# Kernel optimization log

Measured on AMD Instinct MI355X. Metric: run time of the kernel, lower is better.

Reference implementation:

```python
import jax, jax.numpy as jnp
import numpy as np

# Thresholds from PointsGeneration.__init__ defaults
THRES_TEXT = 0.45
THRES_HEAD = 0.5
THRES_BOND = 0.5

H = W = 2048


def setup_inputs() -> dict:
    key = jax.random.key(0)
    ks = jax.random.split(key, 7)
    mk = lambda k, c: jax.random.normal(k, (1, c, H, W), dtype=jnp.float32)
    return {
        "score_text": mk(ks[0], 1),
        "score_head": mk(ks[1], 1),
        "score_tail": mk(ks[2], 1),
        "score_bond": mk(ks[3], 1),
        "reg_head": mk(ks[4], 4),
        "reg_tail": mk(ks[5], 4),
        "reg_bond": mk(ks[6], 4),
    }


def reference(score_text, score_head, score_tail, score_bond, reg_head, reg_tail, reg_bond):
    # Sigmoid activations (exactly as in torch forward).
    s_text = jax.nn.sigmoid(score_text)
    s_head = jax.nn.sigmoid(score_head)
    s_tail = jax.nn.sigmoid(score_tail)
    s_bond = jax.nn.sigmoid(score_bond)

    # Per-pixel thresholding performed by the .so before per-instance point
    # generation: center-text mask, head/tail masks (within text region),
    # pixels passing the corresponding mask, so we gate them here.
    m_text = (s_text > THRES_TEXT).astype(s_text.dtype)   # [1,1,H,W]
    m_head = m_text * (s_head > THRES_HEAD).astype(s_head.dtype)
    m_tail = m_text * (s_tail > THRES_HEAD).astype(s_tail.dtype)
    m_bond = (s_bond > THRES_BOND).astype(s_bond.dtype)

    gated = jnp.concatenate([
        reg_head * m_head,   # [1,4,H,W]
        reg_tail * m_tail,   # [1,4,H,W]
        reg_bond * m_bond,   # [1,4,H,W]
    ], axis=1)

    return jnp.concatenate([s_text, s_head, s_tail, s_bond, gated], axis=1)
```

## Files before the change

kernel.cpp:

```cpp
#include <hip/hip_runtime.h>
#include <math.h>


static __device__ __forceinline__ float sigf(float x) {
    return 1.0f / (1.0f + expf(-x));
}

__global__ __launch_bounds__(256) void points_gen_kernel(
    const float* __restrict__ p_text,
    const float* __restrict__ p_head,
    const float* __restrict__ p_tail,
    const float* __restrict__ p_bond,
    const float* __restrict__ p_rh,
    const float* __restrict__ p_rt,
    const float* __restrict__ p_rb,
    float* __restrict__ out)
{
    constexpr int N = 2048 * 2048;
    const int t = blockIdx.x * blockDim.x + threadIdx.x;
    const int i = t * 4;

    float4 ft = *reinterpret_cast<const float4*>(p_text + i);
    float4 fh = *reinterpret_cast<const float4*>(p_head + i);
    float4 fl = *reinterpret_cast<const float4*>(p_tail + i);
    float4 fb = *reinterpret_cast<const float4*>(p_bond + i);

    float st[4] = {ft.x, ft.y, ft.z, ft.w};
    float sh[4] = {fh.x, fh.y, fh.z, fh.w};
    float sl[4] = {fl.x, fl.y, fl.z, fl.w};
    float sb[4] = {fb.x, fb.y, fb.z, fb.w};

    float mh[4], ml[4], mb[4];
#pragma unroll
    for (int k = 0; k < 4; ++k) {
        st[k] = sigf(st[k]);
        sh[k] = sigf(sh[k]);
        sl[k] = sigf(sl[k]);
        sb[k] = sigf(sb[k]);
        const float mt = (st[k] > 0.45f) ? 1.0f : 0.0f;
        mh[k] = (sh[k] > 0.5f) ? mt : 0.0f;
        ml[k] = (sl[k] > 0.5f) ? mt : 0.0f;
        mb[k] = (sb[k] > 0.5f) ? 1.0f : 0.0f;
    }

    *reinterpret_cast<float4*>(out + 0 * N + i) = make_float4(st[0], st[1], st[2], st[3]);
    *reinterpret_cast<float4*>(out + 1 * N + i) = make_float4(sh[0], sh[1], sh[2], sh[3]);
    *reinterpret_cast<float4*>(out + 2 * N + i) = make_float4(sl[0], sl[1], sl[2], sl[3]);
    *reinterpret_cast<float4*>(out + 3 * N + i) = make_float4(sb[0], sb[1], sb[2], sb[3]);

#pragma unroll
    for (int c = 0; c < 4; ++c) {
        float4 v = *reinterpret_cast<const float4*>(p_rh + c * N + i);
        v.x *= mh[0]; v.y *= mh[1]; v.z *= mh[2]; v.w *= mh[3];
        *reinterpret_cast<float4*>(out + (4 + c) * N + i) = v;
    }
#pragma unroll
    for (int c = 0; c < 4; ++c) {
        float4 v = *reinterpret_cast<const float4*>(p_rt + c * N + i);
        v.x *= ml[0]; v.y *= ml[1]; v.z *= ml[2]; v.w *= ml[3];
        *reinterpret_cast<float4*>(out + (8 + c) * N + i) = v;
    }
#pragma unroll
    for (int c = 0; c < 4; ++c) {
        float4 v = *reinterpret_cast<const float4*>(p_rb + c * N + i);
        v.x *= mb[0]; v.y *= mb[1]; v.z *= mb[2]; v.w *= mb[3];
        *reinterpret_cast<float4*>(out + (12 + c) * N + i) = v;
    }
}

extern "C" void kernel_launch(void* const* d_in, const int* in_sizes, int n_in,
                              void* d_out, int out_size, void* d_ws, size_t ws_size,
                              hipStream_t stream) {
    (void)in_sizes; (void)n_in; (void)out_size; (void)d_ws; (void)ws_size;

    const float* p_text = (const float*)d_in[0];
    const float* p_head = (const float*)d_in[1];
    const float* p_tail = (const float*)d_in[2];
    const float* p_bond = (const float*)d_in[3];
    const float* p_rh   = (const float*)d_in[4];
    const float* p_rt   = (const float*)d_in[5];
    const float* p_rb   = (const float*)d_in[6];
    float* out = (float*)d_out;

    constexpr int N = 2048 * 2048;
    constexpr int threads = 256;
    constexpr int n4 = N / 4;
    constexpr int blocks = n4 / threads;

    points_gen_kernel<<<blocks, threads, 0, stream>>>(
        p_text, p_head, p_tail, p_bond, p_rh, p_rt, p_rb, out);
}
```

Measured before the change: 120.7 us.

## Split work into four block groups per output channel set

Each pixel chunk is now processed by four blocks instead of one: one writes the sigmoid maps, and the other three each handle one gated regression group. This raises parallelism and memory-level concurrency with less work per thread. In exchange, the text, head and tail score inputs are re-read by several blocks and their sigmoids are recomputed, adding some redundant traffic. The bond score is read twice.

Result: no change. 120.0 us (-0.6%).

```diff
diff --git a/kernel.cpp b/kernel.cpp
--- a/kernel.cpp
+++ b/kernel.cpp
@@ -4,6 +4,13 @@
 
 static __device__ __forceinline__ float sigf(float x) {
     return 1.0f / (1.0f + expf(-x));
+}
+
+static __device__ __forceinline__ float4 ld4(const float* p) {
+    return *reinterpret_cast<const float4*>(p);
+}
+static __device__ __forceinline__ void st4(float* p, float4 v) {
+    *reinterpret_cast<float4*>(p) = v;
 }
 
 __global__ __launch_bounds__(256) void points_gen_kernel(
@@ -17,54 +24,71 @@
     float* __restrict__ out)
 {
     constexpr int N = 2048 * 2048;
-    const int t = blockIdx.x * blockDim.x + threadIdx.x;
-    const int i = t * 4;
+    const int bid = blockIdx.x;
+    const int g = bid & 3;
+    const int i = ((bid >> 2) * 256 + threadIdx.x) * 4;
 
-    float4 ft = *reinterpret_cast<const float4*>(p_text + i);
-    float4 fh = *reinterpret_cast<const float4*>(p_head + i);
-    float4 fl = *reinterpret_cast<const float4*>(p_tail + i);
-    float4 fb = *reinterpret_cast<const float4*>(p_bond + i);
-
-    float st[4] = {ft.x, ft.y, ft.z, ft.w};
-    float sh[4] = {fh.x, fh.y, fh.z, fh.w};
-    float sl[4] = {fl.x, fl.y, fl.z, fl.w};
-    float sb[4] = {fb.x, fb.y, fb.z, fb.w};
-
-    float mh[4], ml[4], mb[4];
+    if (g == 0) {
+        float4 ft = ld4(p_text + i);
+        float4 fh = ld4(p_head + i);
+        float4 fl = ld4(p_tail + i);
+        float4 fb = ld4(p_bond + i);
+        float* t = &ft.x; float* h = &fh.x; float* l = &fl.x; float* b = &fb.x;
 #pragma unroll
-    for (int k = 0; k < 4; ++k) {
-        st[k] = sigf(st[k]);
-        sh[k] = sigf(sh[k]);
-        sl[k] = sigf(sl[k]);
-        sb[k] = sigf(sb[k]);
-        const float mt = (st[k] > 0.45f) ? 1.0f : 0.0f;
-        mh[k] = (sh[k] > 0.5f) ? mt : 0.0f;
-        ml[k] = (sl[k] > 0.5f) ? mt : 0.0f;
-        mb[k] = (sb[k] > 0.5f) ? 1.0f : 0.0f;
-    }
-
-    *reinterpret_cast<float4*>(out + 0 * N + i) = make_float4(st[0], st[1], st[2], st[3]);
-    *reinterpret_cast<float4*>(out + 1 * N + i) = make_float4(sh[0], sh[1], sh[2], sh[3]);
-    *reinterpret_cast<float4*>(out + 2 * N + i) = make_float4(sl[0], sl[1], sl[2], sl[3]);
-    *reinterpret_cast<float4*>(out + 3 * N + i) = make_float4(sb[0], sb[1], sb[2], sb[3]);
-
+        for (int k = 0; k < 4; ++k) {
+            t[k] = sigf(t[k]); h[k] = sigf(h[k]);
+            l[k] = sigf(l[k]); b[k] = sigf(b[k]);
+        }
+        st4(out + 0 * N + i, ft);
+        st4(out + 1 * N + i, fh);
+        st4(out + 2 * N + i, fl);
+        st4(out + 3 * N + i, fb);
+    } else if (g == 1) {
+        float4 ft = ld4(p_text + i);
+        float4 fh = ld4(p_head + i);
+        const float* t = &ft.x; const float* h = &fh.x;
+        float m[4];
 #pragma unroll
-    for (int c = 0; c < 4; ++c) {
-        float4 v = *reinterpret_cast<const float4*>(p_rh + c * N + i);
-        v.x *= mh[0]; v.y *= mh[1]; v.z *= mh[2]; v.w *= mh[3];
-        *reinterpret_cast<float4*>(out + (4 + c) * N + i) = v;
-    }
+        for (int k = 0; k < 4; ++k) {
+            const float mt = (sigf(t[k]) > 0.45f) ? 1.0f : 0.0f;
+            m[k] = (sigf(h[k]) > 0.5f) ? mt : 0.0f;
+        }
 #pragma unroll
-    for (int c = 0; c < 4; ++c) {
-        float4 v = *reinterpret_cast<const float4*>(p_rt + c * N + i);
-        v.x *= ml[0]; v.y *= ml[1]; v.z *= ml[2]; v.w *= ml[3];
-        *reinterpret_cast<float4*>(out + (8 + c) * N + i) = v;
-    }
+        for (int c = 0; c < 4; ++c) {
+            float4 v = ld4(p_rh + c * N + i);
+            v.x *= m[0]; v.y *= m[1]; v.z *= m[2]; v.w *= m[3];
+            st4(out + (4 + c) * N + i, v);
+        }
+    } else if (g == 2) {
+        float4 ft = ld4(p_text + i);
+        float4 fl = ld4(p_tail + i);
+        const float* t = &ft.x; const float* l = &fl.x;
+        float m[4];
 #pragma unroll
-    for (int c = 0; c < 4; ++c) {
-        float4 v = *reinterpret_cast<const float4*>(p_rb + c * N + i);
-        v.x *= mb[0]; v.y *= mb[1]; v.z *= mb[2]; v.w *= mb[3];
-        *reinterpret_cast<float4*>(out + (12 + c) * N + i) = v;
+        for (int k = 0; k < 4; ++k) {
+            const float mt = (sigf(t[k]) > 0.45f) ? 1.0f : 0.0f;
+            m[k] = (sigf(l[k]) > 0.5f) ? mt : 0.0f;
+        }
+#pragma unroll
+        for (int c = 0; c < 4; ++c) {
+            float4 v = ld4(p_rt + c * N + i);
+            v.x *= m[0]; v.y *= m[1]; v.z *= m[2]; v.w *= m[3];
+            st4(out + (8 + c) * N + i, v);
+        }
+    } else {
+        float4 fb = ld4(p_bond + i);
+        const float* b = &fb.x;
+        float m[4];
+#pragma unroll
+        for (int k = 0; k < 4; ++k) {
+            m[k] = (sigf(b[k]) > 0.5f) ? 1.0f : 0.0f;
+        }
+#pragma unroll
+        for (int c = 0; c < 4; ++c) {
+            float4 v = ld4(p_rb + c * N + i);
+            v.x *= m[0]; v.y *= m[1]; v.z *= m[2]; v.w *= m[3];
+            st4(out + (12 + c) * N + i, v);
+        }
     }
 }
 
@@ -85,7 +109,8 @@
     constexpr int N = 2048 * 2048;
     constexpr int threads = 256;
     constexpr int n4 = N / 4;
-    constexpr int blocks = n4 / threads;
+    constexpr int blocks_per_group = n4 / threads;
+    constexpr int blocks = blocks_per_group * 4;
 
     points_gen_kernel<<<blocks, threads, 0, stream>>>(
         p_text, p_head, p_tail, p_bond, p_rh, p_rt, p_rb, out);
```
